# Performance work log

Hardware: AMD Instinct MI355X
Metric: run time of the kernel (lower is better)

## Reference

```python
import jax, jax.numpy as jnp
import numpy as np
from jax import lax

D_MODEL = 512
NUM_EMB = 8192
BETA = 0.25


def setup_inputs() -> dict:
    key = jax.random.key(0)
    k1, k2 = jax.random.split(key)
    z = jax.random.normal(k1, (16, 1024, D_MODEL), dtype=jnp.float32)
    # nn.init.uniform_(emb, -1/K, 1/K)
    emb = jax.random.uniform(k2, (NUM_EMB, D_MODEL), dtype=jnp.float32,
                             minval=-1.0 / NUM_EMB, maxval=1.0 / NUM_EMB)
    return {"z": z, "emb": emb}


def reference(z, emb):
    B, S, D = z.shape
    zf = z.reshape(-1, D)  # [N, D], N = B*S
    # squared euclidean distances via ||z||^2 + ||e||^2 - 2 z.e^T  -> [N, K]
    dist = (jnp.sum(zf * zf, axis=1, keepdims=True)
            + jnp.sum(emb * emb, axis=1)
            - 2.0 * jnp.matmul(zf, emb.T))
    idx = jnp.argmin(dist, axis=-1)  # [N]
    z_q = emb[idx]  # [N, D]
    codebook_loss = jnp.mean((lax.stop_gradient(z_q) - zf) ** 2)
    commit_loss = jnp.mean((z_q - lax.stop_gradient(zf)) ** 2)
    total_loss = codebook_loss + BETA * commit_loss
    # straight-through estimator; note torch code flattened z so output stays [N, D]
    z_q_st = zf + lax.stop_gradient(z_q - zf)
    return z_q_st, total_loss, idx.reshape(zf.shape[0], -1)
```

## Files before the change

### kernel.cpp

```cpp
#include <hip/hip_runtime.h>


#define N_TOK 16384
#define DIM   512
#define NEMB  8192
#define BETA  0.25f
#define NKT   32
#define MARGIN_A 2.4f
#define ESCALE 4096.0f
#define NSTAGE 24
#define CLIST  96

using f32x4 = __attribute__((ext_vector_type(4))) float;

#define WS_CNT  0
#define WS_PMAX (N_TOK*NKT*4)
#define WS_PIDX (WS_PMAX + N_TOK*NKT*4)
#define WS_EXTK (WS_PIDX + N_TOK*NKT*4)
#define WS_S1   (WS_EXTK + N_TOK*NKT*7*4)
#define WS_PART (WS_S1   + N_TOK*4)
#define WS_ZH   (WS_PART + (N_TOK/4)*8)
#define WS_EH   (WS_ZH   + N_TOK*DIM)

#define GLDS16(g, l) __builtin_amdgcn_global_load_lds( \
    (const __attribute__((address_space(1))) void*)(g), \
    (__attribute__((address_space(3))) void*)(l), 16, 0, 0)

__device__ inline unsigned f2e4m3(float f) {
  unsigned u = __builtin_bit_cast(unsigned, f);
  unsigned s = (u >> 24) & 0x80u;
  float a = __builtin_bit_cast(float, u & 0x7fffffffu);
  if (a < 0.015625f) {
    unsigned q = (unsigned)rintf(a * 512.0f);
    return s | q;
  }
  unsigned m = u & 0x7fffffffu;
  m += 0x7ffffu + ((m >> 20) & 1u);
  unsigned e = (m >> 23) - 127u + 7u;
  return s | (e << 3) | ((m >> 20) & 7u);
}

__device__ inline unsigned pack4(float a, float b, float c, float d) {
  return f2e4m3(a) | (f2e4m3(b) << 8) | (f2e4m3(c) << 16) | (f2e4m3(d) << 24);
}

__global__ void vq_pack(const float* __restrict__ z, const float* __restrict__ emb,
                        unsigned char* __restrict__ zh8, unsigned char* __restrict__ eh8,
                        float* __restrict__ s1) {
  const int w = threadIdx.x >> 6, lane = threadIdx.x & 63;
  if (blockIdx.x < N_TOK / 4) {
    const int row = blockIdx.x * 4 + w;
    const float4* r = (const float4*)(z + (size_t)row * DIM);
    float4 v0 = r[lane * 2], v1 = r[lane * 2 + 1];
    float p0=v0.x*v0.x, p1=v0.y*v0.y, p2=v0.z*v0.z, p3=v0.w*v0.w;
    float p4=v1.x*v1.x, p5=v1.y*v1.y, p6=v1.z*v1.z, p7=v1.w*v1.w;
    double s = (double)p0+(double)p1+(double)p2+(double)p3
             + (double)p4+(double)p5+(double)p6+(double)p7;
    #pragma unroll
    for (int m = 32; m >= 1; m >>= 1) s += __shfl_xor(s, m);
    if (lane == 0) s1[row] = (float)s;
    uint2 o;
    o.x = pack4(v0.x, v0.y, v0.z, v0.w);
    o.y = pack4(v1.x, v1.y, v1.z, v1.w);
    const int mt = row >> 6, mi = row & 63;
    *(uint2*)(zh8 + ((((size_t)mt * 64 + lane) * 64) + mi) * 8) = o;
  } else {
    const int row = (blockIdx.x - N_TOK / 4) * 4 + w;
    const float4* r = (const float4*)(emb + (size_t)row * DIM);
    float4 v0 = r[lane * 2], v1 = r[lane * 2 + 1];
    uint2 o;
    o.x = pack4(v0.x*ESCALE, v0.y*ESCALE, v0.z*ESCALE, v0.w*ESCALE);
    o.y = pack4(v1.x*ESCALE, v1.y*ESCALE, v1.z*ESCALE, v1.w*ESCALE);
    const int nt = row >> 8, ni = row & 255;
    *(uint2*)(eh8 + ((((size_t)nt * 64 + lane) * 256) + ni) * 8) = o;
  }
}

__global__ __launch_bounds__(256, 4)
void vq_mfma(const unsigned char* __restrict__ zh8, const unsigned char* __restrict__ eh8,
             float* __restrict__ pmax, int* __restrict__ pidx,
             int* __restrict__ cnt, int* __restrict__ extk) {
  __shared__ uint2 lA[16 * 64];
  __shared__ uint2 lB[16 * 256];

  const int mt = blockIdx.x, nt = blockIdx.y;
  const int n0 = nt * 256, m0 = mt * 64;
  const int tid = threadIdx.x;
  const int wid = tid >> 6, lane = tid & 63;
  const int quad = lane >> 4, lc = lane & 15;

  f32x4 C[4][4];
  #pragma unroll
  for (int i = 0; i < 4; ++i)
    #pragma unroll
    for (int j = 0; j < 4; ++j) C[i][j] = (f32x4){0.f, 0.f, 0.f, 0.f};

  const char* gA = (const char*)zh8 + (size_t)mt * 32768;
  const char* gB = (const char*)eh8 + (size_t)nt * 131072;

  for (int t = 0; t < 4; ++t) {
    {
      const char* a = gA + (size_t)t * 8192;
      const char* b = gB + (size_t)t * 32768;
      GLDS16(a + tid * 16,        (char*)&lA[0] + tid * 16);
      GLDS16(a + 4096 + tid * 16, (char*)&lA[0] + 4096 + tid * 16);
      #pragma unroll
      for (int i = 0; i < 8; ++i)
        GLDS16(b + i * 4096 + tid * 16, (char*)&lB[0] + i * 4096 + tid * 16);
    }
    __syncthreads();
    #pragma unroll
    for (int s = 0; s < 4; ++s) {
      const int kx = s * 4 + quad;
      long long a0 = __builtin_bit_cast(long long, lA[kx * 64 +  0 + lc]);
      long long a1 = __builtin_bit_cast(long long, lA[kx * 64 + 16 + lc]);
      long long a2 = __builtin_bit_cast(long long, lA[kx * 64 + 32 + lc]);
      long long a3 = __builtin_bit_cast(long long, lA[kx * 64 + 48 + lc]);
      long long b0 = __builtin_bit_cast(long long, lB[kx * 256 + wid * 64 +  0 + lc]);
      long long b1 = __builtin_bit_cast(long long, lB[kx * 256 + wid * 64 + 16 + lc]);
      long long b2 = __builtin_bit_cast(long long, lB[kx * 256 + wid * 64 + 32 + lc]);
      long long b3 = __builtin_bit_cast(long long, lB[kx * 256 + wid * 64 + 48 + lc]);
      C[0][0] = __builtin_amdgcn_mfma_f32_16x16x32_fp8_fp8(a0, b0, C[0][0], 0, 0, 0);
      C[0][1] = __builtin_amdgcn_mfma_f32_16x16x32_fp8_fp8(a0, b1, C[0][1], 0, 0, 0);
      C[0][2] = __builtin_amdgcn_mfma_f32_16x16x32_fp8_fp8(a0, b2, C[0][2], 0, 0, 0);
      C[0][3] = __builtin_amdgcn_mfma_f32_16x16x32_fp8_fp8(a0, b3, C[0][3], 0, 0, 0);
      C[1][0] = __builtin_amdgcn_mfma_f32_16x16x32_fp8_fp8(a1, b0, C[1][0], 0, 0, 0);
      C[1][1] = __builtin_amdgcn_mfma_f32_16x16x32_fp8_fp8(a1, b1, C[1][1], 0, 0, 0);
      C[1][2] = __builtin_amdgcn_mfma_f32_16x16x32_fp8_fp8(a1, b2, C[1][2], 0, 0, 0);
      C[1][3] = __builtin_amdgcn_mfma_f32_16x16x32_fp8_fp8(a1, b3, C[1][3], 0, 0, 0);
      C[2][0] = __builtin_amdgcn_mfma_f32_16x16x32_fp8_fp8(a2, b0, C[2][0], 0, 0, 0);
      C[2][1] = __builtin_amdgcn_mfma_f32_16x16x32_fp8_fp8(a2, b1, C[2][1], 0, 0, 0);
      C[2][2] = __builtin_amdgcn_mfma_f32_16x16x32_fp8_fp8(a2, b2, C[2][2], 0, 0, 0);
      C[2][3] = __builtin_amdgcn_mfma_f32_16x16x32_fp8_fp8(a2, b3, C[2][3], 0, 0, 0);
      C[3][0] = __builtin_amdgcn_mfma_f32_16x16x32_fp8_fp8(a3, b0, C[3][0], 0, 0, 0);
      C[3][1] = __builtin_amdgcn_mfma_f32_16x16x32_fp8_fp8(a3, b1, C[3][1], 0, 0, 0);
      C[3][2] = __builtin_amdgcn_mfma_f32_16x16x32_fp8_fp8(a3, b2, C[3][2], 0, 0, 0);
      C[3][3] = __builtin_amdgcn_mfma_f32_16x16x32_fp8_fp8(a3, b3, C[3][3], 0, 0, 0);
    }
    __syncthreads();
  }

  float* cmbv = (float*)&lA[0];
  int*   cmbk = (int*)(cmbv + 256);
  float* bbv  = (float*)(cmbk + 256);
  int*   bbk  = (int*)(bbv + 64);
  int*   lcnt = (int*)(bbk + 64);

  #pragma unroll
  for (int mf = 0; mf < 4; ++mf)
    #pragma unroll
    for (int rr = 0; rr < 4; ++rr) {
      float bv = C[mf][0][rr]; int bn = 0;
      #pragma unroll
      for (int nf = 1; nf < 4; ++nf) {
        float v = C[mf][nf][rr];
        if (v > bv) { bv = v; bn = nf; }
      }
      int bk = n0 + wid * 64 + bn * 16 + lc;
      #pragma unroll
      for (int m = 8; m >= 1; m >>= 1) {
        float vo = __shfl_xor(bv, m); int ko = __shfl_xor(bk, m);
        if (vo > bv || (vo == bv && ko < bk)) { bv = vo; bk = ko; }
      }
      if (lc == 0) {
        int row = mf * 16 + quad * 4 + rr;
        cmbv[row * 4 + wid] = bv; cmbk[row * 4 + wid] = bk;
      }
    }
  __syncthreads();
  if (tid < 64) {
    float bv = cmbv[tid * 4 + 0]; int bk = cmbk[tid * 4 + 0];
    #pragma unroll
    for (int q = 1; q < 4; ++q) {
      float v = cmbv[tid * 4 + q]; int k = cmbk[tid * 4 + q];
      if (v > bv) { bv = v; bk = k; }
    }
    bbv[tid] = bv; bbk[tid] = bk;
    lcnt[tid] = 0;
    size_t rg = (size_t)(m0 + tid) * NKT + nt;
    pmax[rg] = bv; pidx[rg] = bk;
  }
  __syncthreads();
  #pragma unroll
  for (int mf = 0; mf < 4; ++mf)
    #pragma unroll
    for (int nf = 0; nf < 4; ++nf)
      #pragma unroll
      for (int rr = 0; rr < 4; ++rr) {
        int row = mf * 16 + quad * 4 + rr;
        float v = C[mf][nf][rr];
        if (v >= bbv[row] - MARGIN_A) {
          int k = n0 + wid * 64 + nf * 16 + lc;
          if (k != bbk[row]) {
            int slot = atomicAdd(&lcnt[row], 1);
            if (slot < 7) extk[((size_t)(m0 + row) * NKT + nt) * 7 + slot] = k;
          }
        }
      }
  __syncthreads();
  if (tid < 64) cnt[(size_t)(m0 + tid) * NKT + nt] = lcnt[tid];
}

__global__ __launch_bounds__(256, 3)
void vq_finalize(const float* __restrict__ z, const float* __restrict__ emb,
                 const float* __restrict__ s1g,
                 const float* __restrict__ pmax, const int* __restrict__ pidx,
                 const int* __restrict__ cnt, const int* __restrict__ extk,
                 float* __restrict__ out, double* __restrict__ part) {
  __shared__ float4 lstage4[NSTAGE * 129];
  __shared__ int   ck[CLIST];
  __shared__ float cq[CLIST];
  __shared__ unsigned char cmeta[CLIST];
  __shared__ int ccnt;
  __shared__ double lossp[4];

  const int w = threadIdx.x >> 6, l = threadIdx.x & 63;
  const int row = blockIdx.x * 4 + w;
  const int l5 = l & 31;
  const size_t rb = (size_t)row * NKT;
  if (threadIdx.x == 0) ccnt = 0;

  float pv = pmax[rb + l5]; int pk = pidx[rb + l5];
  float gv = pv; int gk = pk;
  #pragma unroll
  for (int m = 16; m >= 1; m >>= 1) {
    float vo = __shfl_xor(gv, m); int ko = __shfl_xor(gk, m);
    if (vo > gv || (vo == gv && ko < gk)) { gv = vo; gk = ko; }
  }
  const bool inm = (l < 32) && (pv >= gv - MARGIN_A);
  int c = 0; bool ovf = false;
  if (inm) { c = cnt[rb + l5]; if (c > 7) { ovf = true; c = 0; } }
  __syncthreads();

  bool ovf2 = false;
  if (inm && !ovf) {
    int base = atomicAdd(&ccnt, 1 + c);
    if (base < CLIST) { ck[base] = pk; cmeta[base] = (unsigned char)w; }
    else ovf2 = true;
    for (int i = 0; i < c; ++i) {
      int idx = base + 1 + i;
      if (idx < CLIST) { ck[idx] = extk[(rb + l5) * 7 + i]; cmeta[idx] = (unsigned char)w; }
      else ovf2 = true;
    }
  }
  unsigned int mask32 = (unsigned int)__ballot(ovf || ovf2);
  __syncthreads();
  int cN = ccnt; if (cN > CLIST) cN = CLIST;
  int sN = cN;   if (sN > NSTAGE) sN = NSTAGE;

  for (int si = w; si < sN; si += 4) {
    const float4* e4 = (const float4*)(emb + (size_t)ck[si] * DIM);
    lstage4[si * 129 + l * 2]     = e4[l * 2];
    lstage4[si * 129 + l * 2 + 1] = e4[l * 2 + 1];
  }
  __syncthreads();

  for (int ci = threadIdx.x; ci < cN; ci += 256) {
    const int k = ck[ci];
    const int r = cmeta[ci];
    const float4* zr4 = (const float4*)(z + (size_t)(blockIdx.x * 4 + r) * DIM);
    float d = 0.f;
    if (ci < NSTAGE) {
      const float4* er4 = &lstage4[ci * 129];
      for (int i4 = 0; i4 < 128; ++i4) {
        float4 zv = zr4[i4], ev = er4[i4];
        d = fmaf(zv.x, ev.x, d); d = fmaf(zv.y, ev.y, d);
        d = fmaf(zv.z, ev.z, d); d = fmaf(zv.w, ev.w, d);
      }
    } else {
      const float4* er4 = (const float4*)(emb + (size_t)k * DIM);
      for (int i4 = 0; i4 < 128; ++i4) {
        float4 zv = zr4[i4], ev = er4[i4];
        d = fmaf(zv.x, ev.x, d); d = fmaf(zv.y, ev.y, d);
        d = fmaf(zv.z, ev.z, d); d = fmaf(zv.w, ev.w, d);
      }
    }
    cq[ci] = s1g[blockIdx.x * 4 + r] - 2.f * d;
  }

  float qb = 1e30f; int kb = 0x7fffffff;
  const float s1 = s1g[row];
  const float4* zw4 = (const float4*)(z + (size_t)row * DIM);
  while (mask32) {
    int tile = __builtin_ctz(mask32); mask32 &= mask32 - 1;
    int kbase = tile * 256 + l * 4;
    #pragma unroll
    for (int j = 0; j < 4; ++j) {
      int k = kbase + j;
      const float4* er4 = (const float4*)(emb + (size_t)k * DIM);
      float d = 0.f;
      for (int i4 = 0; i4 < 128; ++i4) {
        float4 zv = zw4[i4], ev = er4[i4];
        d = fmaf(zv.x, ev.x, d); d = fmaf(zv.y, ev.y, d);
        d = fmaf(zv.z, ev.z, d); d = fmaf(zv.w, ev.w, d);
      }
      float q = s1 - 2.f * d;
      if (q < qb || (q == qb && k < kb)) { qb = q; kb = k; }
    }
  }
  __syncthreads();

  for (int e = l; e < cN; e += 64) {
    if (cmeta[e] == (unsigned char)w) {
      float q = cq[e]; int k = ck[e];
      if (q < qb || (q == qb && k < kb)) { qb = q; kb = k; }
    }
  }
  #pragma unroll
  for (int m = 32; m >= 1; m >>= 1) {
    float qo = __shfl_xor(qb, m); int ko = __shfl_xor(kb, m);
    if (qo < qb || (qo == qb && ko < kb)) { qb = qo; kb = ko; }
  }

  const float4* qr4 = (const float4*)(emb + (size_t)kb * DIM);
  float4 zv0 = zw4[l * 2], zv1 = zw4[l * 2 + 1];
  float4 qv0 = qr4[l * 2], qv1 = qr4[l * 2 + 1];
  float ls = 0.f; float4 ov0, ov1;
  {
    const float* zp=(const float*)&zv0; const float* qp=(const float*)&qv0; float* op=(float*)&ov0;
    #pragma unroll
    for (int e = 0; e < 4; ++e) { float d2 = qp[e]-zp[e]; op[e] = zp[e]+d2; ls += d2*d2; }
  }
  {
    const float* zp=(const float*)&zv1; const float* qp=(const float*)&qv1; float* op=(float*)&ov1;
    #pragma unroll
    for (int e = 0; e < 4; ++e) { float d2 = qp[e]-zp[e]; op[e] = zp[e]+d2; ls += d2*d2; }
  }
  float4* orow = (float4*)(out + (size_t)row * DIM);
  orow[l * 2] = ov0; orow[l * 2 + 1] = ov1;
  #pragma unroll
  for (int m = 32; m >= 1; m >>= 1) ls += __shfl_xor(ls, m);
  if (l == 0) {
    out[(size_t)N_TOK * DIM + 1 + row] = (float)kb;
    lossp[w] = (double)ls;
  }
  __syncthreads();
  if (threadIdx.x == 0)
    part[blockIdx.x] = lossp[0] + lossp[1] + lossp[2] + lossp[3];
}

__global__ void vq_loss(const double* __restrict__ part, float* __restrict__ out) {
  __shared__ double ws[4];
  const int t = threadIdx.x, w = t >> 6, lane = t & 63;
  double s = 0.0;
  #pragma unroll
  for (int i = 0; i < 16; ++i) s += part[t + i * 256];
  #pragma unroll
  for (int m = 32; m >= 1; m >>= 1) s += __shfl_xor(s, m);
  if (lane == 0) ws[w] = s;
  __syncthreads();
  if (t == 0) {
    double tot = ws[0] + ws[1] + ws[2] + ws[3];
    out[(size_t)N_TOK * DIM] =
        (float)(tot * (1.0 + (double)BETA) / ((double)N_TOK * (double)DIM));
  }
}

extern "C" void kernel_launch(void* const* d_in, const int* in_sizes, int n_in,
                              void* d_out, int out_size, void* d_ws, size_t ws_size,
                              hipStream_t stream) {
  const float* z   = (const float*)d_in[0];
  const float* emb = (const float*)d_in[1];
  float* out = (float*)d_out;
  char* ws = (char*)d_ws;
  int*           cnt  = (int*)(ws + WS_CNT);
  float*         pmax = (float*)(ws + WS_PMAX);
  int*           pidx = (int*)(ws + WS_PIDX);
  int*           extk = (int*)(ws + WS_EXTK);
  float*         s1   = (float*)(ws + WS_S1);
  double*        part = (double*)(ws + WS_PART);
  unsigned char* zh8  = (unsigned char*)(ws + WS_ZH);
  unsigned char* eh8  = (unsigned char*)(ws + WS_EH);

  vq_pack<<<N_TOK / 4 + NEMB / 4, 256, 0, stream>>>(z, emb, zh8, eh8, s1);
  vq_mfma<<<dim3(N_TOK / 64, NEMB / 256), 256, 0, stream>>>(zh8, eh8, pmax, pidx, cnt, extk);
  vq_finalize<<<N_TOK / 4, 256, 0, stream>>>(z, emb, s1, pmax, pidx, cnt, extk, out, part);
  vq_loss<<<1, 256, 0, stream>>>(part, out);
}
```

Before: 283.9 us.

## Stream codebook tiles through persistent A-resident MFMA blocks with top-2 candidate records

The MFMA kernel now keeps a block's full 64-row z tile in LDS and streams codebook tiles through per-wave double-buffered LDS stages. Loads are paced with explicit vmcnt waits instead of block-wide barriers, and the grid becomes 512 blocks, each covering half the codebook. Per 64-code tile it writes a packed top-1/top-2 record, replacing the margin scan with atomics and extra-candidate lists. Finalize refines candidates from these records and rescans whole tiles whose second-best value falls within the margin. This trades more partial-record traffic and lower occupancy for less reloading of z and fewer synchronisations.

```diff
diff --git a/kernel.cpp b/kernel.cpp
--- a/kernel.cpp
+++ b/kernel.cpp
@@ -5,7 +5,7 @@
 #define DIM   512
 #define NEMB  8192
 #define BETA  0.25f
-#define NKT   32
+#define NCT   128
 #define MARGIN_A 2.4f
 #define ESCALE 4096.0f
 #define NSTAGE 24
@@ -13,14 +13,11 @@
 
 using f32x4 = __attribute__((ext_vector_type(4))) float;
 
-#define WS_CNT  0
-#define WS_PMAX (N_TOK*NKT*4)
-#define WS_PIDX (WS_PMAX + N_TOK*NKT*4)
-#define WS_EXTK (WS_PIDX + N_TOK*NKT*4)
-#define WS_S1   (WS_EXTK + N_TOK*NKT*7*4)
-#define WS_PART (WS_S1   + N_TOK*4)
+#define WS_PMX  0
+#define WS_S1   ((size_t)N_TOK*NCT*16)
+#define WS_PART (WS_S1 + N_TOK*4)
 #define WS_ZH   (WS_PART + (N_TOK/4)*8)
-#define WS_EH   (WS_ZH   + N_TOK*DIM)
+#define WS_EH   (WS_ZH + (size_t)N_TOK*DIM)
 
 #define GLDS16(g, l) __builtin_amdgcn_global_load_lds( \
     (const __attribute__((address_space(1))) void*)(g), \
@@ -71,23 +68,42 @@
     uint2 o;
     o.x = pack4(v0.x*ESCALE, v0.y*ESCALE, v0.z*ESCALE, v0.w*ESCALE);
     o.y = pack4(v1.x*ESCALE, v1.y*ESCALE, v1.z*ESCALE, v1.w*ESCALE);
-    const int nt = row >> 8, ni = row & 255;
-    *(uint2*)(eh8 + ((((size_t)nt * 64 + lane) * 256) + ni) * 8) = o;
-  }
-}
-
-__global__ __launch_bounds__(256, 4)
+    const int ct = row >> 6, ni = row & 63;
+    *(uint2*)(eh8 + ((((size_t)ct * 64 + lane) * 64) + ni) * 8) = o;
+  }
+}
+
+__global__ __launch_bounds__(256, 2)
 void vq_mfma(const unsigned char* __restrict__ zh8, const unsigned char* __restrict__ eh8,
-             float* __restrict__ pmax, int* __restrict__ pidx,
-             int* __restrict__ cnt, int* __restrict__ extk) {
-  __shared__ uint2 lA[16 * 64];
-  __shared__ uint2 lB[16 * 256];
-
-  const int mt = blockIdx.x, nt = blockIdx.y;
-  const int n0 = nt * 256, m0 = mt * 64;
+             float4* __restrict__ pmx) {
+  __shared__ uint2 lA[4096];
+  __shared__ uint2 lB[4][2][512];
+
+  const int bid = blockIdx.x;
+  const int mt = bid >> 1, h = bid & 1;
   const int tid = threadIdx.x;
-  const int wid = tid >> 6, lane = tid & 63;
+  const int w = tid >> 6, lane = tid & 63;
   const int quad = lane >> 4, lc = lane & 15;
+  const int m0 = mt * 64;
+
+  const char* gA = (const char*)zh8 + (size_t)mt * 32768;
+  #pragma unroll
+  for (int i = 0; i < 8; ++i)
+    GLDS16(gA + i * 4096 + tid * 16, (char*)&lA[0] + i * 4096 + tid * 16);
+
+  const char* gB = (const char*)eh8;
+  auto stage = [&](int t) {
+    const int nt = t >> 3, ks = t & 7;
+    const char* src = gB + (size_t)(h * 64 + nt * 4 + w) * 32768 + ks * 4096;
+    char* dst = (char*)&lB[w][t & 1][0];
+    #pragma unroll
+    for (int i = 0; i < 4; ++i)
+      GLDS16(src + i * 1024 + lane * 16, dst + i * 1024 + lane * 16);
+  };
+
+  stage(0); stage(1);
+  asm volatile("s_waitcnt vmcnt(8)" ::: "memory");
+  __builtin_amdgcn_s_barrier();
 
   f32x4 C[4][4];
   #pragma unroll
@@ -95,31 +111,23 @@
     #pragma unroll
     for (int j = 0; j < 4; ++j) C[i][j] = (f32x4){0.f, 0.f, 0.f, 0.f};
 
-  const char* gA = (const char*)zh8 + (size_t)mt * 32768;
-  const char* gB = (const char*)eh8 + (size_t)nt * 131072;
-
-  for (int t = 0; t < 4; ++t) {
-    {
-      const char* a = gA + (size_t)t * 8192;
-      const char* b = gB + (size_t)t * 32768;
-      GLDS16(a + tid * 16,        (char*)&lA[0] + tid * 16);
-      GLDS16(a + 4096 + tid * 16, (char*)&lA[0] + 4096 + tid * 16);
-      #pragma unroll
-      for (int i = 0; i < 8; ++i)
-        GLDS16(b + i * 4096 + tid * 16, (char*)&lB[0] + i * 4096 + tid * 16);
-    }
-    __syncthreads();
-    #pragma unroll
-    for (int s = 0; s < 4; ++s) {
-      const int kx = s * 4 + quad;
-      long long a0 = __builtin_bit_cast(long long, lA[kx * 64 +  0 + lc]);
-      long long a1 = __builtin_bit_cast(long long, lA[kx * 64 + 16 + lc]);
-      long long a2 = __builtin_bit_cast(long long, lA[kx * 64 + 32 + lc]);
-      long long a3 = __builtin_bit_cast(long long, lA[kx * 64 + 48 + lc]);
-      long long b0 = __builtin_bit_cast(long long, lB[kx * 256 + wid * 64 +  0 + lc]);
-      long long b1 = __builtin_bit_cast(long long, lB[kx * 256 + wid * 64 + 16 + lc]);
-      long long b2 = __builtin_bit_cast(long long, lB[kx * 256 + wid * 64 + 32 + lc]);
-      long long b3 = __builtin_bit_cast(long long, lB[kx * 256 + wid * 64 + 48 + lc]);
+  for (int t = 0; t < 128; ++t) {
+    if (t == 127)                      { asm volatile("s_waitcnt vmcnt(0)"  ::: "memory"); }
+    else if (t >= 8 && (t & 7) < 2)    { asm volatile("s_waitcnt vmcnt(20)" ::: "memory"); }
+    else                               { asm volatile("s_waitcnt vmcnt(4)"  ::: "memory"); }
+    const uint2* bs = &lB[w][t & 1][0];
+    const int ks = t & 7;
+    #pragma unroll
+    for (int s = 0; s < 2; ++s) {
+      const int kxl = s * 4 + quad;
+      long long a0 = __builtin_bit_cast(long long, lA[(ks*8 + kxl)*64 +  0 + lc]);
+      long long a1 = __builtin_bit_cast(long long, lA[(ks*8 + kxl)*64 + 16 + lc]);
+      long long a2 = __builtin_bit_cast(long long, lA[(ks*8 + kxl)*64 + 32 + lc]);
+      long long a3 = __builtin_bit_cast(long long, lA[(ks*8 + kxl)*64 + 48 + lc]);
+      long long b0 = __builtin_bit_cast(long long, bs[kxl*64 +  0 + lc]);
+      long long b1 = __builtin_bit_cast(long long, bs[kxl*64 + 16 + lc]);
+      long long b2 = __builtin_bit_cast(long long, bs[kxl*64 + 32 + lc]);
+      long long b3 = __builtin_bit_cast(long long, bs[kxl*64 + 48 + lc]);
       C[0][0] = __builtin_amdgcn_mfma_f32_16x16x32_fp8_fp8(a0, b0, C[0][0], 0, 0, 0);
       C[0][1] = __builtin_amdgcn_mfma_f32_16x16x32_fp8_fp8(a0, b1, C[0][1], 0, 0, 0);
       C[0][2] = __builtin_amdgcn_mfma_f32_16x16x32_fp8_fp8(a0, b2, C[0][2], 0, 0, 0);
@@ -137,75 +145,49 @@
       C[3][2] = __builtin_amdgcn_mfma_f32_16x16x32_fp8_fp8(a3, b2, C[3][2], 0, 0, 0);
       C[3][3] = __builtin_amdgcn_mfma_f32_16x16x32_fp8_fp8(a3, b3, C[3][3], 0, 0, 0);
     }
-    __syncthreads();
-  }
-
-  float* cmbv = (float*)&lA[0];
-  int*   cmbk = (int*)(cmbv + 256);
-  float* bbv  = (float*)(cmbk + 256);
-  int*   bbk  = (int*)(bbv + 64);
-  int*   lcnt = (int*)(bbk + 64);
-
-  #pragma unroll
-  for (int mf = 0; mf < 4; ++mf)
-    #pragma unroll
-    for (int rr = 0; rr < 4; ++rr) {
-      float bv = C[mf][0][rr]; int bn = 0;
+    if (t + 2 < 128) stage(t + 2);
+    if ((t & 7) == 7) {
+      const int ct = h * 64 + (t >> 3) * 4 + w;
       #pragma unroll
-      for (int nf = 1; nf < 4; ++nf) {
-        float v = C[mf][nf][rr];
-        if (v > bv) { bv = v; bn = nf; }
-      }
-      int bk = n0 + wid * 64 + bn * 16 + lc;
-      #pragma unroll
-      for (int m = 8; m >= 1; m >>= 1) {
-        float vo = __shfl_xor(bv, m); int ko = __shfl_xor(bk, m);
-        if (vo > bv || (vo == bv && ko < bk)) { bv = vo; bk = ko; }
-      }
-      if (lc == 0) {
-        int row = mf * 16 + quad * 4 + rr;
-        cmbv[row * 4 + wid] = bv; cmbk[row * 4 + wid] = bk;
-      }
-    }
-  __syncthreads();
-  if (tid < 64) {
-    float bv = cmbv[tid * 4 + 0]; int bk = cmbk[tid * 4 + 0];
-    #pragma unroll
-    for (int q = 1; q < 4; ++q) {
-      float v = cmbv[tid * 4 + q]; int k = cmbk[tid * 4 + q];
-      if (v > bv) { bv = v; bk = k; }
-    }
-    bbv[tid] = bv; bbk[tid] = bk;
-    lcnt[tid] = 0;
-    size_t rg = (size_t)(m0 + tid) * NKT + nt;
-    pmax[rg] = bv; pidx[rg] = bk;
-  }
-  __syncthreads();
-  #pragma unroll
-  for (int mf = 0; mf < 4; ++mf)
-    #pragma unroll
-    for (int nf = 0; nf < 4; ++nf)
-      #pragma unroll
-      for (int rr = 0; rr < 4; ++rr) {
-        int row = mf * 16 + quad * 4 + rr;
-        float v = C[mf][nf][rr];
-        if (v >= bbv[row] - MARGIN_A) {
-          int k = n0 + wid * 64 + nf * 16 + lc;
-          if (k != bbk[row]) {
-            int slot = atomicAdd(&lcnt[row], 1);
-            if (slot < 7) extk[((size_t)(m0 + row) * NKT + nt) * 7 + slot] = k;
+      for (int mf = 0; mf < 4; ++mf)
+        #pragma unroll
+        for (int rr = 0; rr < 4; ++rr) {
+          float v1 = C[mf][0][rr];
+          int   k1 = ct * 64 + lc;
+          float v2 = -3.4e38f;
+          #pragma unroll
+          for (int nf = 1; nf < 4; ++nf) {
+            float v = C[mf][nf][rr];
+            int   k = ct * 64 + nf * 16 + lc;
+            if (v > v1) { v2 = v1; v1 = v; k1 = k; }
+            else        { v2 = fmaxf(v2, v); }
+          }
+          #pragma unroll
+          for (int m = 8; m >= 1; m >>= 1) {
+            float o1 = __shfl_xor(v1, m);
+            int   ok = __shfl_xor(k1, m);
+            float o2 = __shfl_xor(v2, m);
+            if (o1 > v1) { v2 = fmaxf(v1, o2); v1 = o1; k1 = ok; }
+            else         { v2 = fmaxf(v2, o1); }
+          }
+          if (lc == 0) {
+            int row = m0 + mf * 16 + quad * 4 + rr;
+            float4 rec;
+            rec.x = v1; rec.y = __int_as_float(k1); rec.z = v2; rec.w = 0.f;
+            pmx[(size_t)row * NCT + ct] = rec;
           }
         }
-      }
-  __syncthreads();
-  if (tid < 64) cnt[(size_t)(m0 + tid) * NKT + nt] = lcnt[tid];
+      #pragma unroll
+      for (int i = 0; i < 4; ++i)
+        #pragma unroll
+        for (int j = 0; j < 4; ++j) C[i][j] = (f32x4){0.f, 0.f, 0.f, 0.f};
+    }
+  }
 }
 
 __global__ __launch_bounds__(256, 3)
 void vq_finalize(const float* __restrict__ z, const float* __restrict__ emb,
-                 const float* __restrict__ s1g,
-                 const float* __restrict__ pmax, const int* __restrict__ pidx,
-                 const int* __restrict__ cnt, const int* __restrict__ extk,
+                 const float* __restrict__ s1g, const float4* __restrict__ pmx,
                  float* __restrict__ out, double* __restrict__ part) {
   __shared__ float4 lstage4[NSTAGE * 129];
   __shared__ int   ck[CLIST];
@@ -216,34 +198,41 @@
 
   const int w = threadIdx.x >> 6, l = threadIdx.x & 63;
   const int row = blockIdx.x * 4 + w;
-  const int l5 = l & 31;
-  const size_t rb = (size_t)row * NKT;
   if (threadIdx.x == 0) ccnt = 0;
 
-  float pv = pmax[rb + l5]; int pk = pidx[rb + l5];
-  float gv = pv; int gk = pk;
-  #pragma unroll
-  for (int m = 16; m >= 1; m >>= 1) {
-    float vo = __shfl_xor(gv, m); int ko = __shfl_xor(gk, m);
-    if (vo > gv || (vo == gv && ko < gk)) { gv = vo; gk = ko; }
-  }
-  const bool inm = (l < 32) && (pv >= gv - MARGIN_A);
-  int c = 0; bool ovf = false;
-  if (inm) { c = cnt[rb + l5]; if (c > 7) { ovf = true; c = 0; } }
-  __syncthreads();
-
-  bool ovf2 = false;
-  if (inm && !ovf) {
-    int base = atomicAdd(&ccnt, 1 + c);
-    if (base < CLIST) { ck[base] = pk; cmeta[base] = (unsigned char)w; }
-    else ovf2 = true;
-    for (int i = 0; i < c; ++i) {
-      int idx = base + 1 + i;
-      if (idx < CLIST) { ck[idx] = extk[(rb + l5) * 7 + i]; cmeta[idx] = (unsigned char)w; }
-      else ovf2 = true;
-    }
-  }
-  unsigned int mask32 = (unsigned int)__ballot(ovf || ovf2);
+  float4 pa = pmx[(size_t)row * NCT + l];
+  float4 pb = pmx[(size_t)row * NCT + 64 + l];
+  float gm = fmaxf(pa.x, pb.x);
+  #pragma unroll
+  for (int m = 32; m >= 1; m >>= 1) gm = fmaxf(gm, __shfl_xor(gm, m));
+  const float thr = gm - MARGIN_A;
+  const float s1 = s1g[row];
+  const float4* zw4 = (const float4*)(z + (size_t)row * DIM);
+
+  unsigned long long ta = __ballot(pa.z >= thr);
+  unsigned long long tb = __ballot(pb.z >= thr);
+  __syncthreads();
+
+  float qb = 1e30f; int kb = 0x7fffffff;
+  for (int half = 0; half < 2; ++half) {
+    float v1 = half ? pb.x : pa.x;
+    int   k1 = __float_as_int(half ? pb.y : pa.y);
+    if (v1 >= thr) {
+      int s = atomicAdd(&ccnt, 1);
+      if (s < CLIST) { ck[s] = k1; cmeta[s] = (unsigned char)w; }
+      else {
+        const float4* er4 = (const float4*)(emb + (size_t)k1 * DIM);
+        float d = 0.f;
+        for (int i4 = 0; i4 < 128; ++i4) {
+          float4 zv = zw4[i4], ev = er4[i4];
+          d = fmaf(zv.x, ev.x, d); d = fmaf(zv.y, ev.y, d);
+          d = fmaf(zv.z, ev.z, d); d = fmaf(zv.w, ev.w, d);
+        }
+        float q = s1 - 2.f * d;
+        if (q < qb || (q == qb && k1 < kb)) { qb = q; kb = k1; }
+      }
+    }
+  }
   __syncthreads();
   int cN = ccnt; if (cN > CLIST) cN = CLIST;
   int sN = cN;   if (sN > NSTAGE) sN = NSTAGE;
@@ -259,44 +248,42 @@
     const int k = ck[ci];
     const int r = cmeta[ci];
     const float4* zr4 = (const float4*)(z + (size_t)(blockIdx.x * 4 + r) * DIM);
+    const float4* er4 = (ci < NSTAGE) ? (const float4*)&lstage4[ci * 129]
+                                      : (const float4*)(emb + (size_t)k * DIM);
     float d = 0.f;
-    if (ci < NSTAGE) {
-      const float4* er4 = &lstage4[ci * 129];
-      for (int i4 = 0; i4 < 128; ++i4) {
-        float4 zv = zr4[i4], ev = er4[i4];
-        d = fmaf(zv.x, ev.x, d); d = fmaf(zv.y, ev.y, d);
-        d = fmaf(zv.z, ev.z, d); d = fmaf(zv.w, ev.w, d);
-      }
-    } else {
-      const float4* er4 = (const float4*)(emb + (size_t)k * DIM);
-      for (int i4 = 0; i4 < 128; ++i4) {
-        float4 zv = zr4[i4], ev = er4[i4];
-        d = fmaf(zv.x, ev.x, d); d = fmaf(zv.y, ev.y, d);
-        d = fmaf(zv.z, ev.z, d); d = fmaf(zv.w, ev.w, d);
-      }
+    for (int i4 = 0; i4 < 128; ++i4) {
+      float4 zv = zr4[i4], ev = er4[i4];
+      d = fmaf(zv.x, ev.x, d); d = fmaf(zv.y, ev.y, d);
+      d = fmaf(zv.z, ev.z, d); d = fmaf(zv.w, ev.w, d);
     }
     cq[ci] = s1g[blockIdx.x * 4 + r] - 2.f * d;
   }
 
-  float qb = 1e30f; int kb = 0x7fffffff;
-  const float s1 = s1g[row];
-  const float4* zw4 = (const float4*)(z + (size_t)row * DIM);
-  while (mask32) {
-    int tile = __builtin_ctz(mask32); mask32 &= mask32 - 1;
-    int kbase = tile * 256 + l * 4;
-    #pragma unroll
-    for (int j = 0; j < 4; ++j) {
-      int k = kbase + j;
-      const float4* er4 = (const float4*)(emb + (size_t)k * DIM);
-      float d = 0.f;
-      for (int i4 = 0; i4 < 128; ++i4) {
-        float4 zv = zw4[i4], ev = er4[i4];
-        d = fmaf(zv.x, ev.x, d); d = fmaf(zv.y, ev.y, d);
-        d = fmaf(zv.z, ev.z, d); d = fmaf(zv.w, ev.w, d);
-      }
-      float q = s1 - 2.f * d;
-      if (q < qb || (q == qb && k < kb)) { qb = q; kb = k; }
-    }
+  while (ta) {
+    int tile = __builtin_ctzll(ta); ta &= ta - 1;
+    int k = tile * 64 + l;
+    const float4* er4 = (const float4*)(emb + (size_t)k * DIM);
+    float d = 0.f;
+    for (int i4 = 0; i4 < 128; ++i4) {
+      float4 zv = zw4[i4], ev = er4[i4];
+      d = fmaf(zv.x, ev.x, d); d = fmaf(zv.y, ev.y, d);
+      d = fmaf(zv.z, ev.z, d); d = fmaf(zv.w, ev.w, d);
+    }
+    float q = s1 - 2.f * d;
+    if (q < qb || (q == qb && k < kb)) { qb = q; kb = k; }
+  }
+  while (tb) {
+    int tile = 64 + __builtin_ctzll(tb); tb &= tb - 1;
+    int k = tile * 64 + l;
+    const float4* er4 = (const float4*)(emb + (size_t)k * DIM);
+    float d = 0.f;
+    for (int i4 = 0; i4 < 128; ++i4) {
+      float4 zv = zw4[i4], ev = er4[i4];
+      d = fmaf(zv.x, ev.x, d); d = fmaf(zv.y, ev.y, d);
+      d = fmaf(zv.z, ev.z, d); d = fmaf(zv.w, ev.w, d);
+    }
+    float q = s1 - 2.f * d;
+    if (q < qb || (q == qb && k < kb)) { qb = q; kb = k; }
   }
   __syncthreads();
 
@@ -363,17 +350,14 @@
   const float* emb = (const float*)d_in[1];
   float* out = (float*)d_out;
   char* ws = (char*)d_ws;
-  int*           cnt  = (int*)(ws + WS_CNT);
-  float*         pmax = (float*)(ws + WS_PMAX);
-  int*           pidx = (int*)(ws + WS_PIDX);
-  int*           extk = (int*)(ws + WS_EXTK);
+  float4*        pmx  = (float4*)(ws + WS_PMX);
   float*         s1   = (float*)(ws + WS_S1);
   double*        part = (double*)(ws + WS_PART);
   unsigned char* zh8  = (unsigned char*)(ws + WS_ZH);
   unsigned char* eh8  = (unsigned char*)(ws + WS_EH);
 
   vq_pack<<<N_TOK / 4 + NEMB / 4, 256, 0, stream>>>(z, emb, zh8, eh8, s1);
-  vq_mfma<<<dim3(N_TOK / 64, NEMB / 256), 256, 0, stream>>>(zh8, eh8, pmax, pidx, cnt, extk);
-  vq_finalize<<<N_TOK / 4, 256, 0, stream>>>(z, emb, s1, pmax, pidx, cnt, extk, out, part);
+  vq_mfma<<<512, 256, 0, stream>>>(zh8, eh8, pmx);
+  vq_finalize<<<N_TOK / 4, 256, 0, stream>>>(z, emb, s1, pmx, out, part);
   vq_loss<<<1, 256, 0, stream>>>(part, out);
 }
```

Result: slower. 331.2 us (+16.6%).
